# Optimization experiments

Measured on AMD Instinct MI355X. Metric: run time of the kernel, lower is better.

## Reference

```python
import jax, jax.numpy as jnp
import numpy as np

N = 50000      # nodes
E = 800000     # edges (before self-loops)
F_IN = 128     # node_feature_dim
H = 128        # hidden_dim
HEADS = 4
DH = H // HEADS
L = 3          # num_layers
OUT = 128      # output_dim
B = 64         # graphs in batch
EPS = 1e-5
NEG_SLOPE = 0.2


def layer_norm(x, g, b):
    mu = jnp.mean(x, axis=-1, keepdims=True)
    var = jnp.mean(jnp.square(x - mu), axis=-1, keepdims=True)
    return (x - mu) * jax.lax.rsqrt(var + EPS) * g + b


def setup_inputs() -> dict:
    key = jax.random.key(0)
    ks = jax.random.split(key, 10)
    s = 0.05
    x = jax.random.normal(ks[0], (N, F_IN), jnp.float32)
    edge_index = jax.random.randint(ks[1], (2, E), 0, N, dtype=jnp.int32)
    batch = jnp.sort(jax.random.randint(ks[2], (N,), 0, B, dtype=jnp.int32))
    return {
        "x": x,
        "edge_index": edge_index,
        "batch": batch,
        # node encoder: Linear + LayerNorm
        "W0": jax.random.normal(ks[3], (F_IN, H), jnp.float32) * s,
        "b0": jnp.zeros((H,), jnp.float32),
        "g0": jnp.ones((H,), jnp.float32),
        "be0": jnp.zeros((H,), jnp.float32),
        # GAT layers (stacked over L)
        "Wg": jax.random.normal(ks[4], (L, H, H), jnp.float32) * s,
        "att_src": jax.random.normal(ks[5], (L, HEADS, DH), jnp.float32) * s,
        "att_dst": jax.random.normal(ks[6], (L, HEADS, DH), jnp.float32) * s,
        "bg": jnp.zeros((L, H), jnp.float32),
        "gg": jnp.ones((L, H), jnp.float32),
        "bgg": jnp.zeros((L, H), jnp.float32),
        # output projection: Linear + LayerNorm
        "Wp": jax.random.normal(ks[7], (H, OUT), jnp.float32) * s,
        "bp": jnp.zeros((OUT,), jnp.float32),
        "gp": jnp.ones((OUT,), jnp.float32),
        "bep": jnp.zeros((OUT,), jnp.float32),
    }


def gnn_forward(x, src, dst, W0, b0, g0, be0, Wg, att_src, att_dst, bg, gg, bgg, Wp, bp, gp, bep, batch):
    n = x.shape[0]
    h = jax.nn.silu(layer_norm(x @ W0 + b0, g0, be0))  # [N, H]
    for l in range(L):
        identity = h
        hh = (h @ Wg[l]).reshape(n, HEADS, DH)                 # [N, heads, dh]
        a_s = jnp.einsum('nhd,hd->nh', hh, att_src[l])         # [N, heads]
        a_d = jnp.einsum('nhd,hd->nh', hh, att_dst[l])
        e = jax.nn.leaky_relu(a_s[src] + a_d[dst], NEG_SLOPE)  # [E', heads]
        m = jax.lax.stop_gradient(jax.ops.segment_max(e, dst, num_segments=n))
        alpha = jnp.exp(e - m[dst])
        denom = jax.ops.segment_sum(alpha, dst, num_segments=n)
        alpha = alpha / denom[dst]                             # segment softmax over dst
        msg = hh[src] * alpha[:, :, None]                      # [E', heads, dh]
        out = jax.ops.segment_sum(msg, dst, num_segments=n).reshape(n, H) + bg[l]
        h = jax.nn.silu(layer_norm(out, gg[l], bgg[l])) + identity
    # global mean pool per graph
    cnt = jax.ops.segment_sum(jnp.ones((n, 1), h.dtype), batch, num_segments=B)
    pooled = jax.ops.segment_sum(h, batch, num_segments=B) / jnp.maximum(cnt, 1.0)
    return jax.nn.silu(layer_norm(pooled @ Wp + bp, gp, bep))  # [B, OUT]


def reference(x, edge_index, batch, W0, b0, g0, be0, Wg, att_src, att_dst, bg, gg, bgg, Wp, bp, gp, bep):
    n = x.shape[0]
    loops = jnp.arange(n, dtype=edge_index.dtype)  # PyG GATConv add_self_loops=True
    src = jnp.concatenate([edge_index[0], loops])
    dst = jnp.concatenate([edge_index[1], loops])
    return gnn_forward(x, src, dst, W0, b0, g0, be0, Wg, att_src, att_dst, bg, gg, bgg, Wp, bp, gp, bep, batch)
```

## Files before the change

### kernel.cpp

```cpp
#include <hip/hip_runtime.h>

#define NN    50000
#define EE    800000
#define EPE   850000
#define NPAD  50048
#define BGR   64
#define NB    98
#define CHUNK 4096
#define NBLK  208
#define BCAP  12288
#define AGCH  64

typedef __attribute__((ext_vector_type(8))) short bf16x8;
typedef __attribute__((ext_vector_type(4))) float f32x4;
typedef __attribute__((ext_vector_type(2))) float f32x2;

__device__ __forceinline__ float bf2f(unsigned short u) {
    return __uint_as_float(((unsigned)u) << 16);
}
__device__ __forceinline__ unsigned short f2bf(float f) {
    unsigned u = __float_as_uint(f);
    unsigned r = (u + 0x7FFFu + ((u >> 16) & 1u)) >> 16;
    return (unsigned short)r;
}
__device__ __forceinline__ float silu(float y) { return y / (1.f + __expf(-y)); }

__global__ __launch_bounds__(256) void pre_kernel(const float* __restrict__ W0,
                                                  const float* __restrict__ Wg,
                                                  unsigned short* __restrict__ WT,
                                                  float* __restrict__ pooled,
                                                  const int* __restrict__ eidx,
                                                  int* __restrict__ hist_blk) {
    __shared__ unsigned short tile[128][129];
    __shared__ int lh[NB];
    int b = blockIdx.x;
    if (b < 4) {
        const float* src = (b == 0) ? W0 : (Wg + (b - 1) * 16384);
        unsigned short* dst = WT + b * 16384;
        for (int i = threadIdx.x; i < 16384; i += 256) tile[i >> 7][i & 127] = f2bf(src[i]);
        __syncthreads();
        for (int i = threadIdx.x; i < 16384; i += 256) {
            int c = i >> 7, k = i & 127;
            dst[i] = tile[k][c];
        }
    } else if (b < 36) {
        int j = (b - 4) * 256 + threadIdx.x;
        pooled[j] = 0.f;
    } else {
        int cb = b - 36;
        for (int t = threadIdx.x; t < NB; t += 256) lh[t] = 0;
        __syncthreads();
        int base = cb * CHUNK;
#pragma unroll
        for (int j = 0; j < CHUNK / 256; ++j) {
            int i = base + j * 256 + threadIdx.x;
            if (i < EPE) {
                int d = (i < EE) ? eidx[EE + i] : (i - EE);
                atomicAdd(&lh[d >> 9], 1);
            }
        }
        __syncthreads();
        for (int t = threadIdx.x; t < NB; t += 256)
            hist_blk[cb * NB + t] = lh[t];
    }
}

__global__ __launch_bounds__(256) void scan_encoder_kernel(
    const int* __restrict__ hist_blk, int* __restrict__ blkOfs, int* __restrict__ bucketBase,
    const float* __restrict__ x, const unsigned short* __restrict__ WT,
    const float* __restrict__ b0, const float* __restrict__ g0,
    const float* __restrict__ be0, unsigned short* __restrict__ h) {
    __shared__ int tot[NB];
    __shared__ int bas[NB];
    if (blockIdx.x == 0) {
        int t = threadIdx.x;
        if (t < NB) {
            int s = 0;
            for (int k = 0; k < NBLK; ++k) s += hist_blk[k * NB + t];
            tot[t] = s;
        }
        __syncthreads();
        if (t == 0) {
            int run = 0;
            for (int b = 0; b < NB; ++b) { bas[b] = run; run += tot[b]; }
            bucketBase[NB] = EPE;
        }
        __syncthreads();
        if (t < NB) {
            int run = bas[t];
            bucketBase[t] = run;
            for (int k = 0; k < NBLK; ++k) {
                blkOfs[k * NB + t] = run;
                run += hist_blk[k * NB + t];
            }
        }
        return;
    }
    int bid = blockIdx.x - 1;
    int wave = threadIdx.x >> 6, lane = threadIdx.x & 63;
    int cl = lane & 15, q = lane >> 4;
    int row0 = bid * 64 + wave * 16;
    int rA = row0 + cl; if (rA >= NN) rA = NN - 1;
    int kq = q * 8;
    f32x4 acc[8];
#pragma unroll
    for (int t = 0; t < 8; ++t) acc[t] = (f32x4){0.f, 0.f, 0.f, 0.f};
#pragma unroll
    for (int k0 = 0; k0 < 128; k0 += 32) {
        const float* xr = x + rA * 128 + k0 + kq;
        f32x4 f0 = *(const f32x4*)(xr);
        f32x4 f1 = *(const f32x4*)(xr + 4);
        bf16x8 a;
#pragma unroll
        for (int j = 0; j < 4; ++j) {
            a[j] = (short)f2bf(f0[j]);
            a[4 + j] = (short)f2bf(f1[j]);
        }
#pragma unroll
        for (int t = 0; t < 8; ++t) {
            bf16x8 b = *(const bf16x8*)(WT + (t * 16 + cl) * 128 + k0 + kq);
            acc[t] = __builtin_amdgcn_mfma_f32_16x16x32_bf16(a, b, acc[t], 0, 0, 0);
        }
    }
    float bcol[8], gcol[8], becol[8];
#pragma unroll
    for (int t = 0; t < 8; ++t) {
        int c = t * 16 + cl;
        bcol[t] = b0[c]; gcol[t] = g0[c]; becol[t] = be0[c];
    }
#pragma unroll
    for (int r = 0; r < 4; ++r) {
        int row = row0 + q * 4 + r;
        float v[8], s = 0.f, ss = 0.f;
#pragma unroll
        for (int t = 0; t < 8; ++t) {
            v[t] = acc[t][r] + bcol[t];
            s += v[t]; ss += v[t] * v[t];
        }
#pragma unroll
        for (int m = 1; m <= 8; m <<= 1) {
            s += __shfl_xor(s, m, 64); ss += __shfl_xor(ss, m, 64);
        }
        float mu = s * (1.f / 128.f);
        float var = ss * (1.f / 128.f) - mu * mu;
        float rstd = rsqrtf(var + 1e-5f);
        if (row < NN) {
#pragma unroll
            for (int t = 0; t < 8; ++t) {
                float y = (v[t] - mu) * rstd * gcol[t] + becol[t];
                h[row * 128 + t * 16 + cl] = f2bf(silu(y));
            }
        }
    }
}

__device__ __forceinline__ void gat_gemm_body(
    int bid, const unsigned short* __restrict__ h, const unsigned short* __restrict__ WT,
    const float* __restrict__ atts, const float* __restrict__ attd,
    unsigned char* __restrict__ hh8, float* __restrict__ a_s, float* __restrict__ a_d,
    float* __restrict__ es) {
    int wave = threadIdx.x >> 6, lane = threadIdx.x & 63;
    int cl = lane & 15, q = lane >> 4;
    int row0 = bid * 64 + wave * 16;
    int rA = row0 + cl; if (rA >= NN) rA = NN - 1;
    int kq = q * 8;
    f32x4 acc[8];
#pragma unroll
    for (int t = 0; t < 8; ++t) acc[t] = (f32x4){0.f, 0.f, 0.f, 0.f};
#pragma unroll
    for (int k0 = 0; k0 < 128; k0 += 32) {
        bf16x8 a = *(const bf16x8*)(h + rA * 128 + k0 + kq);
#pragma unroll
        for (int t = 0; t < 8; ++t) {
            bf16x8 b = *(const bf16x8*)(WT + (t * 16 + cl) * 128 + k0 + kq);
            acc[t] = __builtin_amdgcn_mfma_f32_16x16x32_bf16(a, b, acc[t], 0, 0, 0);
        }
    }
#pragma unroll
    for (int r = 0; r < 4; ++r) {
        int row = row0 + q * 4 + r;
        if (row < NN) {
#pragma unroll
            for (int t = 0; t < 8; ++t) {
                unsigned pk = (unsigned)__builtin_amdgcn_cvt_pk_fp8_f32(acc[t][r], acc[t][r], 0, false);
                int c = t * 16 + cl;
                hh8[row * 128 + ((c & 31) << 2) + (c >> 5)] = (unsigned char)(pk & 0xFFu);
            }
        }
    }
    float as_lo[4], as_hi[4], ad_lo[4], ad_hi[4];
#pragma unroll
    for (int hd = 0; hd < 4; ++hd) {
        as_lo[hd] = atts[hd * 32 + cl];      as_hi[hd] = atts[hd * 32 + 16 + cl];
        ad_lo[hd] = attd[hd * 32 + cl];      ad_hi[hd] = attd[hd * 32 + 16 + cl];
    }
#pragma unroll
    for (int r = 0; r < 4; ++r) {
        int row = row0 + q * 4 + r;
        float ps[4], pd[4];
#pragma unroll
        for (int hd = 0; hd < 4; ++hd) {
            float v0 = acc[2 * hd][r], v1 = acc[2 * hd + 1][r];
            ps[hd] = v0 * as_lo[hd] + v1 * as_hi[hd];
            pd[hd] = v0 * ad_lo[hd] + v1 * ad_hi[hd];
        }
#pragma unroll
        for (int m = 1; m <= 8; m <<= 1) {
#pragma unroll
            for (int hd = 0; hd < 4; ++hd) {
                ps[hd] += __shfl_xor(ps[hd], m, 64);
                pd[hd] += __shfl_xor(pd[hd], m, 64);
            }
        }
        if (row < NN && cl < 4) {
            float vs = (cl == 0) ? ps[0] : (cl == 1) ? ps[1] : (cl == 2) ? ps[2] : ps[3];
            float vd = (cl == 0) ? pd[0] : (cl == 1) ? pd[1] : (cl == 2) ? pd[2] : pd[3];
            a_s[row * 4 + cl] = vs;
            a_d[row * 4 + cl] = vd;
            float e = vs + vd;
            es[row * 4 + cl] = (e > 0.f) ? e : 0.2f * e;
        }
    }
}

__global__ __launch_bounds__(256) void gemm_gat(
    const unsigned short* __restrict__ h, const unsigned short* __restrict__ WT,
    const float* __restrict__ atts, const float* __restrict__ attd,
    unsigned char* __restrict__ hh8, float* __restrict__ a_s, float* __restrict__ a_d,
    float* __restrict__ es) {
    gat_gemm_body(blockIdx.x, h, WT, atts, attd, hh8, a_s, a_d, es);
}

__global__ __launch_bounds__(256) void bin_gat_kernel(
    const int* __restrict__ eidx, const int* __restrict__ blkOfs,
    unsigned* __restrict__ binned,
    const unsigned short* __restrict__ h, const unsigned short* __restrict__ WT1,
    const float* __restrict__ atts, const float* __restrict__ attd,
    unsigned char* __restrict__ hh8, float* __restrict__ a_s, float* __restrict__ a_d,
    float* __restrict__ es) {
    __shared__ unsigned staged[CHUNK];
    __shared__ int lhist[NB];
    __shared__ int lscan[NB];
    __shared__ int cnt2[NB];
    __shared__ int gofs[NB];
    if (blockIdx.x >= NBLK) {
        gat_gemm_body(blockIdx.x - NBLK, h, WT1, atts, attd, hh8, a_s, a_d, es);
        return;
    }
    int cb = blockIdx.x;
    int tid = threadIdx.x;
    for (int t = tid; t < NB; t += 256) { lhist[t] = 0; cnt2[t] = 0; }
    __syncthreads();
    int base = cb * CHUNK;
    unsigned pk[CHUNK / 256];
#pragma unroll
    for (int j = 0; j < CHUNK / 256; ++j) {
        int i = base + j * 256 + tid;
        pk[j] = 0xFFFFFFFFu;
        if (i < EPE) {
            int s, d;
            if (i < EE) { s = eidx[i]; d = eidx[EE + i]; } else { s = i - EE; d = i - EE; }
            pk[j] = ((unsigned)s << 16) | (unsigned)d;
            atomicAdd(&lhist[d >> 9], 1);
        }
    }
    __syncthreads();
    if (tid == 0) {
        int run = 0;
        for (int b = 0; b < NB; ++b) { lscan[b] = run; run += lhist[b]; }
    }
    __syncthreads();
#pragma unroll
    for (int j = 0; j < CHUNK / 256; ++j) {
        if (pk[j] != 0xFFFFFFFFu) {
            int b = (int)((pk[j] & 0xFFFFu) >> 9);
            int lp = lscan[b] + atomicAdd(&cnt2[b], 1);
            staged[lp] = pk[j];
        }
    }
    for (int t = tid; t < NB; t += 256) gofs[t] = blkOfs[cb * NB + t];
    __syncthreads();
    int nTot = lscan[NB - 1] + lhist[NB - 1];
    for (int i = tid; i < nTot; i += 256) {
        unsigned p = staged[i];
        int b = (int)((p & 0xFFFFu) >> 9);
        binned[gofs[b] + (i - lscan[b])] = p;
    }
}

__global__ __launch_bounds__(256) void build_csr(const unsigned* __restrict__ binned,
                                                 const int* __restrict__ bucketBase,
                                                 int* __restrict__ offs,
                                                 int* __restrict__ csr) {
    __shared__ int lcsr[BCAP];
    __shared__ int lcnt[512];
    __shared__ int lofs[512];
    __shared__ int lcur[512];
    __shared__ int psum[256];
    int b = blockIdx.x, tid = threadIdx.x;
    int n0 = b * 512;
    int o0 = bucketBase[b];
    int nTot = bucketBase[b + 1] - o0;
    if (nTot > BCAP) nTot = BCAP;
    for (int j = tid; j < 512; j += 256) lcnt[j] = 0;
    __syncthreads();
    for (int i = tid; i < nTot; i += 256)
        atomicAdd(&lcnt[binned[o0 + i] & 511u], 1);
    __syncthreads();
    int a0 = lcnt[2 * tid], a1 = lcnt[2 * tid + 1];
    psum[tid] = a0 + a1;
    __syncthreads();
    for (int d = 1; d < 256; d <<= 1) {
        int v = (tid >= d) ? psum[tid - d] : 0;
        __syncthreads(); psum[tid] += v; __syncthreads();
    }
    int exclPair = psum[tid] - (a0 + a1);
    lofs[2 * tid] = exclPair;
    lofs[2 * tid + 1] = exclPair + a0;
    lcur[2 * tid] = exclPair;
    lcur[2 * tid + 1] = exclPair + a0;
    __syncthreads();
    for (int j = tid; j < 512; j += 256) {
        int node = n0 + j;
        if (node < NN) offs[node] = o0 + lofs[j];
    }
    if (b == 0 && tid == 0) offs[NN] = EPE;
    for (int i = tid; i < nTot; i += 256) {
        unsigned p = binned[o0 + i];
        int pos = atomicAdd(&lcur[p & 511u], 1);
        if (pos < BCAP) lcsr[pos] = (int)(p >> 16);
    }
    __syncthreads();
    for (int i = tid; i < nTot; i += 256)
        csr[o0 + i] = lcsr[i];
}

__global__ __launch_bounds__(256) void gat_aggregate(
    const int* __restrict__ offs, const int* __restrict__ csr,
    const float* __restrict__ a_s, const float* __restrict__ a_d,
    const float* __restrict__ es, const unsigned char* __restrict__ hh8,
    unsigned short* __restrict__ h,
    const float* __restrict__ bg, const float* __restrict__ gg,
    const float* __restrict__ bgg) {
    __shared__ int   lss[8][AGCH];
    __shared__ f32x4 lww[8][AGCH];
    int wv = threadIdx.x >> 6;
    int lane = threadIdx.x & 63;
    int half = lane >> 5;
    int l32 = lane & 31;
    int ns = wv * 2 + half;
    int node = blockIdx.x * 8 + ns;
    int e0 = offs[node], e1 = offs[node + 1];
    f32x4 ad4 = *(const f32x4*)(a_d + node * 4);
    f32x4 e4  = *(const f32x4*)(es  + node * 4);
    f32x4 dacc = (f32x4){0.f, 0.f, 0.f, 0.f};
    f32x4 xacc = (f32x4){0.f, 0.f, 0.f, 0.f};
    const unsigned char* hp = hh8 + l32 * 4;
    for (int base = e0; base < e1; base += AGCH) {
        int cend = min(e1, base + AGCH);
        int n = cend - base;
        for (int e = base + l32; e < cend; e += 32) {
            int s = csr[e];
            f32x4 as = *(const f32x4*)(a_s + s * 4);
            f32x4 w;
#pragma unroll
            for (int k = 0; k < 4; ++k) {
                float qq = as[k] + ad4[k];
                qq = (qq > 0.f) ? qq : 0.2f * qq;
                w[k] = __expf(qq - e4[k]);
                dacc[k] += w[k];
            }
            lss[ns][e - base] = s;
            lww[ns][e - base] = w;
        }
        asm volatile("s_waitcnt lgkmcnt(0)" ::: "memory");
        int j = 0;
        for (; j + 4 <= n; j += 4) {
            int s0 = lss[ns][j],     s1 = lss[ns][j + 1];
            int s2 = lss[ns][j + 2], s3 = lss[ns][j + 3];
            f32x4 w0 = lww[ns][j],     w1 = lww[ns][j + 1];
            f32x4 w2 = lww[ns][j + 2], w3 = lww[ns][j + 3];
            unsigned v0 = *(const unsigned*)(hp + ((long)s0 << 7));
            unsigned v1 = *(const unsigned*)(hp + ((long)s1 << 7));
            unsigned v2 = *(const unsigned*)(hp + ((long)s2 << 7));
            unsigned v3 = *(const unsigned*)(hp + ((long)s3 << 7));
            f32x2 lo0 = __builtin_amdgcn_cvt_pk_f32_fp8(v0, false);
            f32x2 hi0 = __builtin_amdgcn_cvt_pk_f32_fp8(v0, true);
            f32x2 lo1 = __builtin_amdgcn_cvt_pk_f32_fp8(v1, false);
            f32x2 hi1 = __builtin_amdgcn_cvt_pk_f32_fp8(v1, true);
            f32x2 lo2 = __builtin_amdgcn_cvt_pk_f32_fp8(v2, false);
            f32x2 hi2 = __builtin_amdgcn_cvt_pk_f32_fp8(v2, true);
            f32x2 lo3 = __builtin_amdgcn_cvt_pk_f32_fp8(v3, false);
            f32x2 hi3 = __builtin_amdgcn_cvt_pk_f32_fp8(v3, true);
            xacc[0] += w0[0] * lo0[0]; xacc[1] += w0[1] * lo0[1];
            xacc[2] += w0[2] * hi0[0]; xacc[3] += w0[3] * hi0[1];
            xacc[0] += w1[0] * lo1[0]; xacc[1] += w1[1] * lo1[1];
            xacc[2] += w1[2] * hi1[0]; xacc[3] += w1[3] * hi1[1];
            xacc[0] += w2[0] * lo2[0]; xacc[1] += w2[1] * lo2[1];
            xacc[2] += w2[2] * hi2[0]; xacc[3] += w2[3] * hi2[1];
            xacc[0] += w3[0] * lo3[0]; xacc[1] += w3[1] * lo3[1];
            xacc[2] += w3[2] * hi3[0]; xacc[3] += w3[3] * hi3[1];
        }
        for (; j < n; ++j) {
            int s0 = lss[ns][j];
            f32x4 w0 = lww[ns][j];
            unsigned v0 = *(const unsigned*)(hp + ((long)s0 << 7));
            f32x2 lo0 = __builtin_amdgcn_cvt_pk_f32_fp8(v0, false);
            f32x2 hi0 = __builtin_amdgcn_cvt_pk_f32_fp8(v0, true);
            xacc[0] += w0[0] * lo0[0]; xacc[1] += w0[1] * lo0[1];
            xacc[2] += w0[2] * hi0[0]; xacc[3] += w0[3] * hi0[1];
        }
        if (cend < e1)
            asm volatile("s_waitcnt lgkmcnt(0)" ::: "memory");
    }
#pragma unroll
    for (int m = 1; m <= 16; m <<= 1) {
#pragma unroll
        for (int k = 0; k < 4; ++k) dacc[k] += __shfl_xor(dacc[k], m, 64);
    }
    float o[4], s = 0.f, ss = 0.f;
#pragma unroll
    for (int k = 0; k < 4; ++k) {
        int c = k * 32 + l32;
        o[k] = xacc[k] / dacc[k] + bg[c];
        s += o[k]; ss += o[k] * o[k];
    }
#pragma unroll
    for (int m = 1; m <= 16; m <<= 1) {
        s += __shfl_xor(s, m, 64); ss += __shfl_xor(ss, m, 64);
    }
    float mu = s * (1.f / 128.f);
    float var = ss * (1.f / 128.f) - mu * mu;
    float rstd = rsqrtf(var + 1e-5f);
#pragma unroll
    for (int k = 0; k < 4; ++k) {
        int c = k * 32 + l32;
        float y = (o[k] - mu) * rstd * gg[c] + bgg[c];
        float r = silu(y) + bf2f(h[node * 128 + c]);
        h[node * 128 + c] = f2bf(r);
    }
}

__global__ void pool_kernel(const unsigned short* __restrict__ h, const int* __restrict__ batch,
                            float* __restrict__ pooled) {
    int c = threadIdx.x;
    int r0 = blockIdx.x * 64;
    int rend = r0 + 64; if (rend > NN) rend = NN;
    int cur = batch[r0];
    float acc = 0.f;
    for (int r = r0; r < rend; ++r) {
        int b = batch[r];
        float v = bf2f(h[r * 128 + c]);
        if (b != cur) {
            atomicAdd(&pooled[cur * 128 + c], acc);
            acc = 0.f; cur = b;
        }
        acc += v;
    }
    atomicAdd(&pooled[cur * 128 + c], acc);
}

__global__ void final_kernel(const float* __restrict__ pooled, const int* __restrict__ batch,
                             const float* __restrict__ Wp, const float* __restrict__ bp,
                             const float* __restrict__ gp, const float* __restrict__ bep,
                             float* __restrict__ out) {
    __shared__ float p[128];
    __shared__ float red[128];
    __shared__ int bounds[2];
    int g = blockIdx.x, c = threadIdx.x;
    if (c == 0) {
        int lo = 0, hi = NN;
        while (lo < hi) { int m = (lo + hi) >> 1; if (batch[m] < g) lo = m + 1; else hi = m; }
        bounds[0] = lo;
        int lo2 = lo, hi2 = NN;
        while (lo2 < hi2) { int m = (lo2 + hi2) >> 1; if (batch[m] < g + 1) lo2 = m + 1; else hi2 = m; }
        bounds[1] = lo2;
    }
    __syncthreads();
    float cnt = (float)(bounds[1] - bounds[0]); if (cnt < 1.f) cnt = 1.f;
    p[c] = pooled[g * 128 + c] / cnt;
    __syncthreads();
    float acc = bp[c];
    for (int k = 0; k < 128; ++k) acc += p[k] * Wp[k * 128 + c];
    red[c] = acc;
    __syncthreads();
    if (c < 64) {
        float s = red[c] + red[c + 64];
#pragma unroll
        for (int m = 1; m <= 32; m <<= 1) s += __shfl_xor(s, m, 64);
        if (c == 0) red[0] = s;
    }
    __syncthreads();
    float mu = red[0] * (1.f / 128.f);
    __syncthreads();
    float dv = acc - mu;
    red[c] = dv * dv;
    __syncthreads();
    if (c < 64) {
        float s = red[c] + red[c + 64];
#pragma unroll
        for (int m = 1; m <= 32; m <<= 1) s += __shfl_xor(s, m, 64);
        if (c == 0) red[0] = s;
    }
    __syncthreads();
    float var = red[0] * (1.f / 128.f);
    float rstd = rsqrtf(var + 1e-5f);
    float y = dv * rstd * gp[c] + bep[c];
    out[g * 128 + c] = silu(y);
}

extern "C" void kernel_launch(void* const* d_in, const int* in_sizes, int n_in,
                              void* d_out, int out_size, void* d_ws, size_t ws_size,
                              hipStream_t stream) {
    const float* x    = (const float*)d_in[0];
    const int*   eidx = (const int*)d_in[1];
    const int*   batch= (const int*)d_in[2];
    const float* W0   = (const float*)d_in[3];
    const float* b0   = (const float*)d_in[4];
    const float* g0   = (const float*)d_in[5];
    const float* be0  = (const float*)d_in[6];
    const float* Wg   = (const float*)d_in[7];
    const float* atts = (const float*)d_in[8];
    const float* attd = (const float*)d_in[9];
    const float* bg   = (const float*)d_in[10];
    const float* gg   = (const float*)d_in[11];
    const float* bgg  = (const float*)d_in[12];
    const float* Wp   = (const float*)d_in[13];
    const float* bp   = (const float*)d_in[14];
    const float* gp   = (const float*)d_in[15];
    const float* bep  = (const float*)d_in[16];

    char* ws = (char*)d_ws;
    size_t off = 0;
    auto alloc = [&](size_t bytes) {
        void* p = ws + off;
        off = (off + bytes + 255) & ~(size_t)255;
        return p;
    };
    unsigned short* h        = (unsigned short*)alloc((size_t)NPAD * 128 * 2);
    unsigned char*  hh8      = (unsigned char*)alloc((size_t)NN * 128);
    float*          a_s      = (float*)alloc((size_t)NN * 4 * 4);
    float*          a_d      = (float*)alloc((size_t)NN * 4 * 4);
    float*          es       = (float*)alloc((size_t)NN * 4 * 4);
    int*            offs     = (int*)alloc((size_t)(NN + 1) * 4);
    int*            csr      = (int*)alloc((size_t)EPE * 4);
    unsigned*       binned   = (unsigned*)alloc((size_t)EPE * 4);
    int*            hist_blk = (int*)alloc((size_t)NBLK * NB * 4);
    int*            blkOfs   = (int*)alloc((size_t)NBLK * NB * 4);
    int*            bktBase  = (int*)alloc((size_t)(NB + 1) * 4);
    unsigned short* WT       = (unsigned short*)alloc(4 * 16384 * 2);
    float*          pooled   = (float*)alloc((size_t)BGR * 128 * 4);

    pre_kernel<<<4 + 32 + NBLK, 256, 0, stream>>>(W0, Wg, WT, pooled, eidx, hist_blk);
    scan_encoder_kernel<<<1 + NPAD / 64, 256, 0, stream>>>(hist_blk, blkOfs, bktBase,
                                                           x, WT, b0, g0, be0, h);
    bin_gat_kernel<<<NBLK + NPAD / 64, 256, 0, stream>>>(eidx, blkOfs, binned,
                                                         h, WT + 16384, atts, attd,
                                                         hh8, a_s, a_d, es);
    build_csr<<<NB, 256, 0, stream>>>(binned, bktBase, offs, csr);

    gat_aggregate<<<NN / 8, 256, 0, stream>>>(offs, csr, a_s, a_d, es, hh8, h,
                                              bg, gg, bgg);
    for (int l = 1; l < 3; ++l) {
        gemm_gat<<<NPAD / 64, 256, 0, stream>>>(h, WT + (l + 1) * 16384,
                                                atts + l * 128, attd + l * 128,
                                                hh8, a_s, a_d, es);
        gat_aggregate<<<NN / 8, 256, 0, stream>>>(offs, csr, a_s, a_d, es, hh8, h,
                                                  bg + l * 128, gg + l * 128,
                                                  bgg + l * 128);
    }
    pool_kernel<<<(NN + 63) / 64, 128, 0, stream>>>(h, batch, pooled);
    final_kernel<<<BGR, 128, 0, stream>>>(pooled, batch, Wp, bp, gp, bep, (float*)d_out);
}
```

Before: 333.5 us.

## Use one wavefront per node in aggregation, fuse mean pooling, halve bucket width

The GAT aggregation now gives each node a full 64-lane wavefront. The edges are split across two half-waves using an interleaved shared-memory layout, and the partial sums are combined with a cross-half shuffle. The final layer's aggregation accumulates its output directly into the pooled buffer with atomics, which removes the separate pool kernel and the last write of h. The edge bucketing moves from 512-node to 256-node buckets, giving twice as many CSR build blocks with smaller shared memory. The risks are more atomic contention on pooled (one atomic per node per channel) and the BCAP limit overflowing on dense buckets.

```diff
diff --git a/kernel.cpp b/kernel.cpp
--- a/kernel.cpp
+++ b/kernel.cpp
@@ -5,15 +5,16 @@
 #define EPE   850000
 #define NPAD  50048
 #define BGR   64
-#define NB    98
+#define NB    196
 #define CHUNK 4096
 #define NBLK  208
-#define BCAP  12288
-#define AGCH  64
+#define BCAP  6144
+#define AGCH  128
 
 typedef __attribute__((ext_vector_type(8))) short bf16x8;
 typedef __attribute__((ext_vector_type(4))) float f32x4;
 typedef __attribute__((ext_vector_type(2))) float f32x2;
+typedef __attribute__((ext_vector_type(4))) int   i32x4;
 
 __device__ __forceinline__ float bf2f(unsigned short u) {
     return __uint_as_float(((unsigned)u) << 16);
@@ -56,7 +57,7 @@
             int i = base + j * 256 + threadIdx.x;
             if (i < EPE) {
                 int d = (i < EE) ? eidx[EE + i] : (i - EE);
-                atomicAdd(&lh[d >> 9], 1);
+                atomicAdd(&lh[d >> 8], 1);
             }
         }
         __syncthreads();
@@ -261,7 +262,7 @@
             int s, d;
             if (i < EE) { s = eidx[i]; d = eidx[EE + i]; } else { s = i - EE; d = i - EE; }
             pk[j] = ((unsigned)s << 16) | (unsigned)d;
-            atomicAdd(&lhist[d >> 9], 1);
+            atomicAdd(&lhist[d >> 8], 1);
         }
     }
     __syncthreads();
@@ -273,7 +274,7 @@
 #pragma unroll
     for (int j = 0; j < CHUNK / 256; ++j) {
         if (pk[j] != 0xFFFFFFFFu) {
-            int b = (int)((pk[j] & 0xFFFFu) >> 9);
+            int b = (int)((pk[j] & 0xFFFFu) >> 8);
             int lp = lscan[b] + atomicAdd(&cnt2[b], 1);
             staged[lp] = pk[j];
         }
@@ -283,7 +284,7 @@
     int nTot = lscan[NB - 1] + lhist[NB - 1];
     for (int i = tid; i < nTot; i += 256) {
         unsigned p = staged[i];
-        int b = (int)((p & 0xFFFFu) >> 9);
+        int b = (int)((p & 0xFFFFu) >> 8);
         binned[gofs[b] + (i - lscan[b])] = p;
     }
 }
@@ -293,41 +294,35 @@
                                                  int* __restrict__ offs,
                                                  int* __restrict__ csr) {
     __shared__ int lcsr[BCAP];
-    __shared__ int lcnt[512];
-    __shared__ int lofs[512];
-    __shared__ int lcur[512];
+    __shared__ int lcnt[256];
+    __shared__ int lcur[256];
     __shared__ int psum[256];
     int b = blockIdx.x, tid = threadIdx.x;
-    int n0 = b * 512;
+    int n0 = b * 256;
     int o0 = bucketBase[b];
     int nTot = bucketBase[b + 1] - o0;
     if (nTot > BCAP) nTot = BCAP;
-    for (int j = tid; j < 512; j += 256) lcnt[j] = 0;
+    lcnt[tid] = 0;
     __syncthreads();
     for (int i = tid; i < nTot; i += 256)
-        atomicAdd(&lcnt[binned[o0 + i] & 511u], 1);
-    __syncthreads();
-    int a0 = lcnt[2 * tid], a1 = lcnt[2 * tid + 1];
-    psum[tid] = a0 + a1;
+        atomicAdd(&lcnt[binned[o0 + i] & 255u], 1);
+    __syncthreads();
+    int a = lcnt[tid];
+    psum[tid] = a;
     __syncthreads();
     for (int d = 1; d < 256; d <<= 1) {
         int v = (tid >= d) ? psum[tid - d] : 0;
         __syncthreads(); psum[tid] += v; __syncthreads();
     }
-    int exclPair = psum[tid] - (a0 + a1);
-    lofs[2 * tid] = exclPair;
-    lofs[2 * tid + 1] = exclPair + a0;
-    lcur[2 * tid] = exclPair;
-    lcur[2 * tid + 1] = exclPair + a0;
-    __syncthreads();
-    for (int j = tid; j < 512; j += 256) {
-        int node = n0 + j;
-        if (node < NN) offs[node] = o0 + lofs[j];
-    }
+    int excl = psum[tid] - a;
+    lcur[tid] = excl;
+    int node = n0 + tid;
+    if (node < NN) offs[node] = o0 + excl;
     if (b == 0 && tid == 0) offs[NN] = EPE;
+    __syncthreads();
     for (int i = tid; i < nTot; i += 256) {
         unsigned p = binned[o0 + i];
-        int pos = atomicAdd(&lcur[p & 511u], 1);
+        int pos = atomicAdd(&lcur[p & 255u], 1);
         if (pos < BCAP) lcsr[pos] = (int)(p >> 16);
     }
     __syncthreads();
@@ -341,15 +336,15 @@
     const float* __restrict__ es, const unsigned char* __restrict__ hh8,
     unsigned short* __restrict__ h,
     const float* __restrict__ bg, const float* __restrict__ gg,
-    const float* __restrict__ bgg) {
-    __shared__ int   lss[8][AGCH];
-    __shared__ f32x4 lww[8][AGCH];
+    const float* __restrict__ bgg,
+    const int* __restrict__ batch, float* __restrict__ pooled, int last) {
+    __shared__ int   lss[4][AGCH];
+    __shared__ f32x4 lww[4][AGCH];
     int wv = threadIdx.x >> 6;
     int lane = threadIdx.x & 63;
-    int half = lane >> 5;
+    int hf = lane >> 5;
     int l32 = lane & 31;
-    int ns = wv * 2 + half;
-    int node = blockIdx.x * 8 + ns;
+    int node = blockIdx.x * 4 + wv;
     int e0 = offs[node], e1 = offs[node + 1];
     f32x4 ad4 = *(const f32x4*)(a_d + node * 4);
     f32x4 e4  = *(const f32x4*)(es  + node * 4);
@@ -359,8 +354,8 @@
     for (int base = e0; base < e1; base += AGCH) {
         int cend = min(e1, base + AGCH);
         int n = cend - base;
-        for (int e = base + l32; e < cend; e += 32) {
-            int s = csr[e];
+        for (int i = lane; i < n; i += 64) {
+            int s = csr[base + i];
             f32x4 as = *(const f32x4*)(a_s + s * 4);
             f32x4 w;
 #pragma unroll
@@ -370,20 +365,23 @@
                 w[k] = __expf(qq - e4[k]);
                 dacc[k] += w[k];
             }
-            lss[ns][e - base] = s;
-            lww[ns][e - base] = w;
+            int slot = ((i & 1) << 6) | (i >> 1);
+            lss[wv][slot] = s;
+            lww[wv][slot] = w;
         }
         asm volatile("s_waitcnt lgkmcnt(0)" ::: "memory");
-        int j = 0;
-        for (; j + 4 <= n; j += 4) {
-            int s0 = lss[ns][j],     s1 = lss[ns][j + 1];
-            int s2 = lss[ns][j + 2], s3 = lss[ns][j + 3];
-            f32x4 w0 = lww[ns][j],     w1 = lww[ns][j + 1];
-            f32x4 w2 = lww[ns][j + 2], w3 = lww[ns][j + 3];
-            unsigned v0 = *(const unsigned*)(hp + ((long)s0 << 7));
-            unsigned v1 = *(const unsigned*)(hp + ((long)s1 << 7));
-            unsigned v2 = *(const unsigned*)(hp + ((long)s2 << 7));
-            unsigned v3 = *(const unsigned*)(hp + ((long)s3 << 7));
+        int cnt = (n - hf + 1) >> 1;
+        const int*   sp = &lss[wv][hf << 6];
+        const f32x4* wp = &lww[wv][hf << 6];
+        int jj = 0;
+        for (; jj + 4 <= cnt; jj += 4) {
+            i32x4 s4 = *(const i32x4*)(sp + jj);
+            f32x4 w0 = wp[jj + 0], w1 = wp[jj + 1];
+            f32x4 w2 = wp[jj + 2], w3 = wp[jj + 3];
+            unsigned v0 = *(const unsigned*)(hp + ((long)s4[0] << 7));
+            unsigned v1 = *(const unsigned*)(hp + ((long)s4[1] << 7));
+            unsigned v2 = *(const unsigned*)(hp + ((long)s4[2] << 7));
+            unsigned v3 = *(const unsigned*)(hp + ((long)s4[3] << 7));
             f32x2 lo0 = __builtin_amdgcn_cvt_pk_f32_fp8(v0, false);
             f32x2 hi0 = __builtin_amdgcn_cvt_pk_f32_fp8(v0, true);
             f32x2 lo1 = __builtin_amdgcn_cvt_pk_f32_fp8(v1, false);
@@ -401,9 +399,9 @@
             xacc[0] += w3[0] * lo3[0]; xacc[1] += w3[1] * lo3[1];
             xacc[2] += w3[2] * hi3[0]; xacc[3] += w3[3] * hi3[1];
         }
-        for (; j < n; ++j) {
-            int s0 = lss[ns][j];
-            f32x4 w0 = lww[ns][j];
+        for (; jj < cnt; ++jj) {
+            int s0 = sp[jj];
+            f32x4 w0 = wp[jj];
             unsigned v0 = *(const unsigned*)(hp + ((long)s0 << 7));
             f32x2 lo0 = __builtin_amdgcn_cvt_pk_f32_fp8(v0, false);
             f32x2 hi0 = __builtin_amdgcn_cvt_pk_f32_fp8(v0, true);
@@ -414,14 +412,16 @@
             asm volatile("s_waitcnt lgkmcnt(0)" ::: "memory");
     }
 #pragma unroll
-    for (int m = 1; m <= 16; m <<= 1) {
+    for (int k = 0; k < 4; ++k) xacc[k] += __shfl_xor(xacc[k], 32, 64);
+#pragma unroll
+    for (int m = 1; m <= 32; m <<= 1) {
 #pragma unroll
         for (int k = 0; k < 4; ++k) dacc[k] += __shfl_xor(dacc[k], m, 64);
     }
     float o[4], s = 0.f, ss = 0.f;
 #pragma unroll
     for (int k = 0; k < 4; ++k) {
-        int c = k * 32 + l32;
+        int c = (k << 5) + l32;
         o[k] = xacc[k] / dacc[k] + bg[c];
         s += o[k]; ss += o[k] * o[k];
     }
@@ -432,32 +432,26 @@
     float mu = s * (1.f / 128.f);
     float var = ss * (1.f / 128.f) - mu * mu;
     float rstd = rsqrtf(var + 1e-5f);
-#pragma unroll
-    for (int k = 0; k < 4; ++k) {
-        int c = k * 32 + l32;
-        float y = (o[k] - mu) * rstd * gg[c] + bgg[c];
-        float r = silu(y) + bf2f(h[node * 128 + c]);
-        h[node * 128 + c] = f2bf(r);
-    }
-}
-
-__global__ void pool_kernel(const unsigned short* __restrict__ h, const int* __restrict__ batch,
-                            float* __restrict__ pooled) {
-    int c = threadIdx.x;
-    int r0 = blockIdx.x * 64;
-    int rend = r0 + 64; if (rend > NN) rend = NN;
-    int cur = batch[r0];
-    float acc = 0.f;
-    for (int r = r0; r < rend; ++r) {
-        int b = batch[r];
-        float v = bf2f(h[r * 128 + c]);
-        if (b != cur) {
-            atomicAdd(&pooled[cur * 128 + c], acc);
-            acc = 0.f; cur = b;
-        }
-        acc += v;
-    }
-    atomicAdd(&pooled[cur * 128 + c], acc);
+    if (hf == 0) {
+        if (last) {
+            int g = batch[node];
+#pragma unroll
+            for (int k = 0; k < 4; ++k) {
+                int c = (k << 5) + l32;
+                float y = (o[k] - mu) * rstd * gg[c] + bgg[c];
+                float r = silu(y) + bf2f(h[node * 128 + c]);
+                atomicAdd(&pooled[g * 128 + c], r);
+            }
+        } else {
+#pragma unroll
+            for (int k = 0; k < 4; ++k) {
+                int c = (k << 5) + l32;
+                float y = (o[k] - mu) * rstd * gg[c] + bgg[c];
+                float r = silu(y) + bf2f(h[node * 128 + c]);
+                h[node * 128 + c] = f2bf(r);
+            }
+        }
+    }
 }
 
 __global__ void final_kernel(const float* __restrict__ pooled, const int* __restrict__ batch,
@@ -559,16 +553,15 @@
                                                          hh8, a_s, a_d, es);
     build_csr<<<NB, 256, 0, stream>>>(binned, bktBase, offs, csr);
 
-    gat_aggregate<<<NN / 8, 256, 0, stream>>>(offs, csr, a_s, a_d, es, hh8, h,
-                                              bg, gg, bgg);
+    gat_aggregate<<<NN / 4, 256, 0, stream>>>(offs, csr, a_s, a_d, es, hh8, h,
+                                              bg, gg, bgg, batch, pooled, 0);
     for (int l = 1; l < 3; ++l) {
         gemm_gat<<<NPAD / 64, 256, 0, stream>>>(h, WT + (l + 1) * 16384,
                                                 atts + l * 128, attd + l * 128,
                                                 hh8, a_s, a_d, es);
-        gat_aggregate<<<NN / 8, 256, 0, stream>>>(offs, csr, a_s, a_d, es, hh8, h,
+        gat_aggregate<<<NN / 4, 256, 0, stream>>>(offs, csr, a_s, a_d, es, hh8, h,
                                                   bg + l * 128, gg + l * 128,
-                                                  bgg + l * 128);
-    }
-    pool_kernel<<<(NN + 63) / 64, 128, 0, stream>>>(h, batch, pooled);
+                                                  bgg + l * 128, batch, pooled, l == 2);
+    }
     final_kernel<<<BGR, 128, 0, stream>>>(pooled, batch, Wp, bp, gp, bep, (float*)d_out);
 }
```

New measurement: 472.8 us. 1.42x slower.
